# Performance work log

Hardware: AMD Instinct MI355X
Metric: run time of the kernel (lower is better)

The kernel has to match this reference:

```python
import jax, jax.numpy as jnp
import numpy as np
import math

VOCAB, D, H, NL, L, B = 50257, 768, 12, 4, 1024, 2
DH = D // H
DFF = 4 * D
ALPHA = 0.25
NEG = -1e9


def _ln(x, g, b, eps=1e-5):
    mu = x.mean(-1, keepdims=True)
    var = ((x - mu) ** 2).mean(-1, keepdims=True)
    return (x - mu) * jax.lax.rsqrt(var + eps) * g + b


def setup_inputs() -> dict:
    key = jax.random.key(0)
    ks = jax.random.split(key, 16)
    s = 0.02
    tokens = jax.random.randint(ks[0], (B, L), 0, VOCAB)
    timelike_mask = jax.random.randint(ks[1], (NL, D), 0, 2).astype(jnp.int32)
    embed = jax.random.normal(ks[2], (VOCAB, D), jnp.float32) * s
    pos_emb = jax.random.normal(ks[3], (L, D), jnp.float32) * s
    wq = jax.random.normal(ks[4], (NL, D, D), jnp.float32) * s
    wk = jax.random.normal(ks[5], (NL, D, D), jnp.float32) * s
    wv = jax.random.normal(ks[6], (NL, D, D), jnp.float32) * s
    wo = jax.random.normal(ks[7], (NL, D, D), jnp.float32) * s
    ff_w1 = jax.random.normal(ks[8], (NL, DFF, D), jnp.float32) * s
    ff_b1 = jnp.zeros((NL, DFF), jnp.float32)
    ff_w2 = jax.random.normal(ks[9], (NL, D, DFF), jnp.float32) * s
    ff_b2 = jnp.zeros((NL, D), jnp.float32)
    ln1_g = jnp.ones((NL, D), jnp.float32); ln1_b = jnp.zeros((NL, D), jnp.float32)
    ln2_g = jnp.ones((NL, D), jnp.float32); ln2_b = jnp.zeros((NL, D), jnp.float32)
    lnf_g = jnp.ones((D,), jnp.float32); lnf_b = jnp.zeros((D,), jnp.float32)
    return dict(tokens=tokens, timelike_mask=timelike_mask, embed=embed, pos_emb=pos_emb,
                wq=wq, wk=wk, wv=wv, wo=wo,
                ln1_g=ln1_g, ln1_b=ln1_b, ln2_g=ln2_g, ln2_b=ln2_b,
                ff_w1=ff_w1, ff_b1=ff_b1, ff_w2=ff_w2, ff_b2=ff_b2,
                lnf_g=lnf_g, lnf_b=lnf_b)


def reference(tokens, timelike_mask, embed, pos_emb, wq, wk, wv, wo,
              ln1_g, ln1_b, ln2_g, ln2_b, ff_w1, ff_b1, ff_w2, ff_b2,
              lnf_g, lnf_b):
    Bc, Lc = tokens.shape
    scale = math.sqrt(DH)
    # embeddings: token + learned position
    h = embed[tokens] + pos_emb[None, :Lc]  # (B,L,D)
    # additive causal mask, matching torch's -inf attention_mask convention
    causal = jnp.where(jnp.tril(jnp.ones((Lc, Lc), bool)), 0.0, NEG)[None, None]  # (1,1,L,L)
    for i in range(NL):
        xn = _ln(h, ln1_g[i], ln1_b[i])
        # nn.Linear(bias=False): y = x @ W.T, W is (out,in)
        q = jnp.einsum('bld,od->blo', xn, wq[i]).reshape(Bc, Lc, H, DH).astype(jnp.float32)
        k = jnp.einsum('bld,od->blo', xn, wk[i]).reshape(Bc, Lc, H, DH).astype(jnp.float32)
        v = jnp.einsum('bld,od->blo', xn, wv[i]).reshape(Bc, Lc, H, DH)
        # Minkowski term: scores_std - 2*alpha*(Q*P_t)K^T  ==  (Q*(1-2*alpha*m)) K^T
        m = timelike_mask[i].astype(jnp.float32).reshape(H, DH)  # per-head timelike directions
        q_eff = q * (1.0 - 2.0 * ALPHA * m)[None, None]
        scores = jnp.einsum('bqhd,bkhd->bhqk', q_eff, k) / scale + causal
        aw = jax.nn.softmax(scores, axis=-1)  # dropout=0 (eval)
        attn = jnp.einsum('bhqk,bkhd->bqhd', aw, v).reshape(Bc, Lc, D)
        h = h + jnp.einsum('bld,od->blo', attn, wo[i])
        xn2 = _ln(h, ln2_g[i], ln2_b[i])
        ff = jax.nn.gelu(jnp.einsum('bld,fd->blf', xn2, ff_w1[i]) + ff_b1[i], approximate=False)
        h = h + jnp.einsum('blf,df->bld', ff, ff_w2[i]) + ff_b2[i]
    h = _ln(h, lnf_g, lnf_b)
    logits = jnp.einsum('bld,vd->blv', h, embed)  # tied LM head
    return logits
```

## Files before the change

kernel.cpp:

```cpp
#include <hip/hip_runtime.h>
#include <math.h>

#define VOCABSZ 50257
#define VPAD 50432
#define DMODEL 768
#define NHEAD 12
#define NLAYER 4
#define SEQ 1024
#define BATCH 2
#define DHEAD 64
#define DFFN 3072
#define BT (BATCH * SEQ)
#define NBH (BATCH * NHEAD)

typedef __attribute__((ext_vector_type(8))) short bf16x8;
typedef __attribute__((ext_vector_type(4))) float f32x4;

__device__ __forceinline__ ushort f2bf(float f) {
  uint u = __builtin_bit_cast(uint, f);
  u = (u + 0x7fffu + ((u >> 16) & 1u)) >> 16;
  return (ushort)u;
}

__device__ __forceinline__ void gl_lds16(const ushort* g, ushort* l) {
  __builtin_amdgcn_global_load_lds(
      (const __attribute__((address_space(1))) void*)g,
      (__attribute__((address_space(3))) void*)l, 16, 0, 0);
}

__global__ __launch_bounds__(256) void conv4_kernel(
    const float* __restrict__ src, ushort* __restrict__ dst, int n4) {
  int i = blockIdx.x * 256 + threadIdx.x;
  if (i >= n4) return;
  float4 v = reinterpret_cast<const float4*>(src)[i];
  reinterpret_cast<ushort4*>(dst)[i] =
      make_ushort4(f2bf(v.x), f2bf(v.y), f2bf(v.z), f2bf(v.w));
}

__global__ __launch_bounds__(256) void conv_qkv_kernel(
    const float* __restrict__ src, ushort* __restrict__ dst, int qoff4) {
  const int per4 = DMODEL * DMODEL / 4;
  int i = blockIdx.x * 256 + threadIdx.x;
  if (i >= NLAYER * per4) return;
  int layer = i / per4, rem = i % per4;
  float4 v = reinterpret_cast<const float4*>(src)[i];
  reinterpret_cast<ushort4*>(dst)[(size_t)layer * (3 * per4) + qoff4 + rem] =
      make_ushort4(f2bf(v.x), f2bf(v.y), f2bf(v.z), f2bf(v.w));
}

__global__ __launch_bounds__(256) void conv_embed_kernel(
    const float* __restrict__ emb, ushort* __restrict__ dst) {
  int i = blockIdx.x * 256 + threadIdx.x;
  if (i >= VPAD * DMODEL / 4) return;
  int row = (i * 4) / DMODEL;
  ushort4 o = make_ushort4(0, 0, 0, 0);
  if (row < VOCABSZ) {
    float4 v = reinterpret_cast<const float4*>(emb)[i];
    o = make_ushort4(f2bf(v.x), f2bf(v.y), f2bf(v.z), f2bf(v.w));
  }
  reinterpret_cast<ushort4*>(dst)[i] = o;
}

__global__ __launch_bounds__(256) void embed_kernel(
    const int* __restrict__ tok, const float* __restrict__ emb,
    const float* __restrict__ pos, float* __restrict__ h) {
  int row = blockIdx.x;
  int l = row % SEQ;
  int t = tok[row];
  int tid = threadIdx.x;
#pragma unroll
  for (int j = 0; j < 3; ++j) {
    int c = tid + j * 256;
    h[(size_t)row * DMODEL + c] =
        emb[(size_t)t * DMODEL + c] + pos[(size_t)l * DMODEL + c];
  }
}

template <int KS, bool RBIAS>
__global__ __launch_bounds__(256) void ln_kernel(
    float* __restrict__ h, const float* __restrict__ part,
    const float* __restrict__ rb, const float* __restrict__ g,
    const float* __restrict__ bta, ushort* __restrict__ o) {
  __shared__ float red[8];
  int row = blockIdx.x;
  int tid = threadIdx.x;
  float* xr = h + (size_t)row * DMODEL;
  float v[3];
  float s = 0.f, sq = 0.f;
#pragma unroll
  for (int j = 0; j < 3; ++j) {
    int c = tid + j * 256;
    float a = xr[c];
    if (RBIAS) a += rb[c];
    if (KS > 0) {
#pragma unroll
      for (int z = 0; z < KS; ++z)
        a += part[(size_t)z * BT * DMODEL + (size_t)row * DMODEL + c];
      xr[c] = a;
    }
    v[j] = a;
    s += a;
    sq += a * a;
  }
#pragma unroll
  for (int off = 1; off < 64; off <<= 1) {
    s += __shfl_xor(s, off);
    sq += __shfl_xor(sq, off);
  }
  int wid = tid >> 6;
  if ((tid & 63) == 0) { red[wid * 2] = s; red[wid * 2 + 1] = sq; }
  __syncthreads();
  float S = red[0] + red[2] + red[4] + red[6];
  float SQ = red[1] + red[3] + red[5] + red[7];
  float mu = S * (1.0f / DMODEL);
  float var = SQ * (1.0f / DMODEL) - mu * mu;
  float r = rsqrtf(var + 1e-5f);
  ushort* orow = o + (size_t)row * DMODEL;
#pragma unroll
  for (int j = 0; j < 3; ++j) {
    int c = tid + j * 256;
    orow[c] = f2bf((v[j] - mu) * r * g[c] + bta[c]);
  }
}

__global__ __launch_bounds__(256) void fattn_kernel(
    const ushort* __restrict__ q, const ushort* __restrict__ k,
    const ushort* __restrict__ vt, ushort* __restrict__ o) {
  __shared__ __align__(16) ushort Ks[64 * 64];
  __shared__ __align__(16) ushort Vs[64 * 64];
  __shared__ __align__(16) ushort Ps[4][16][80];
  const int z = blockIdx.y, b = z / NHEAD, hh = z % NHEAD;
  const int q0 = (gridDim.x - 1 - blockIdx.x) * 64;
  const int tid = threadIdx.x, w = tid >> 6, l = tid & 63;
  const int fr = l & 15, ks = l >> 4;
  const int qrow = q0 + w * 16 + fr;
  const ushort* qp = q + (size_t)(b * SEQ + qrow) * DMODEL + hh * DHEAD;
  const bf16x8 qf0 = *reinterpret_cast<const bf16x8*>(qp + ks * 8);
  const bf16x8 qf1 = *reinterpret_cast<const bf16x8*>(qp + 32 + ks * 8);

  const int srow = w * 16 + (l >> 3);
  const int sslot = l & 7;

  f32x4 acc_o[4] = {};
  float mrun = -1e30f, lrun = 0.f;

  for (int k0 = 0; k0 <= q0; k0 += 64) {
#pragma unroll
    for (int c = 0; c < 2; ++c) {
      int r = srow + c * 8;
      int g = sslot ^ (r & 7);
      gl_lds16(k + (size_t)(b * SEQ + k0 + r) * DMODEL + hh * DHEAD + g * 8,
               Ks + (w * 16 + c * 8) * 64);
      gl_lds16(vt + (size_t)(z * 64 + r) * SEQ + k0 + g * 8,
               Vs + (w * 16 + c * 8) * 64);
    }
    __syncthreads();
    f32x4 acc_s[4] = {};
#pragma unroll
    for (int kstep = 0; kstep < 2; ++kstep) {
      const bf16x8 qf = kstep ? qf1 : qf0;
#pragma unroll
      for (int kb = 0; kb < 4; ++kb) {
        int ra = kb * 16 + fr;
        bf16x8 af = *reinterpret_cast<const bf16x8*>(
            Ks + ra * 64 + (((kstep * 4 + ks) ^ (ra & 7)) * 8));
        acc_s[kb] =
            __builtin_amdgcn_mfma_f32_16x16x32_bf16(af, qf, acc_s[kb], 0, 0, 0);
      }
    }
    const bool diag = (k0 == q0);
    float pm = -1e30f;
    float sv[4][4];
#pragma unroll
    for (int kb = 0; kb < 4; ++kb)
#pragma unroll
      for (int r = 0; r < 4; ++r) {
        float s = acc_s[kb][r];
        if (diag && (k0 + kb * 16 + ks * 4 + r > qrow)) s = -1e30f;
        sv[kb][r] = s;
        pm = fmaxf(pm, s);
      }
    pm = fmaxf(pm, __shfl_xor(pm, 16));
    pm = fmaxf(pm, __shfl_xor(pm, 32));
    float mnew = fmaxf(mrun, pm);
    float scale = __expf(mrun - mnew);
    float psum = 0.f;
#pragma unroll
    for (int kb = 0; kb < 4; ++kb) {
      float p0 = __expf(sv[kb][0] - mnew);
      float p1 = __expf(sv[kb][1] - mnew);
      float p2 = __expf(sv[kb][2] - mnew);
      float p3 = __expf(sv[kb][3] - mnew);
      psum += (p0 + p1) + (p2 + p3);
      *reinterpret_cast<ushort4*>(&Ps[w][fr][kb * 16 + ks * 4]) =
          make_ushort4(f2bf(p0), f2bf(p1), f2bf(p2), f2bf(p3));
    }
    psum += __shfl_xor(psum, 16);
    psum += __shfl_xor(psum, 32);
    lrun = lrun * scale + psum;
    mrun = mnew;
#pragma unroll
    for (int db = 0; db < 4; ++db) acc_o[db] *= scale;
#pragma unroll
    for (int kstep = 0; kstep < 2; ++kstep) {
      bf16x8 pf =
          *reinterpret_cast<const bf16x8*>(&Ps[w][fr][kstep * 32 + ks * 8]);
#pragma unroll
      for (int db = 0; db < 4; ++db) {
        int rd = db * 16 + fr;
        bf16x8 vf = *reinterpret_cast<const bf16x8*>(
            Vs + rd * 64 + (((kstep * 4 + ks) ^ (rd & 7)) * 8));
        acc_o[db] =
            __builtin_amdgcn_mfma_f32_16x16x32_bf16(vf, pf, acc_o[db], 0, 0, 0);
      }
    }
    __syncthreads();
  }
  float rinv = 1.0f / lrun;
#pragma unroll
  for (int db = 0; db < 4; ++db) {
    ushort4 o4 =
        make_ushort4(f2bf(acc_o[db][0] * rinv), f2bf(acc_o[db][1] * rinv),
                     f2bf(acc_o[db][2] * rinv), f2bf(acc_o[db][3] * rinv));
    *reinterpret_cast<ushort4*>(o + (size_t)(b * SEQ + qrow) * DMODEL +
                                hh * DHEAD + db * 16 + ks * 4) = o4;
  }
}

template <bool QKV, bool BIAS, bool GELU, bool RES, bool OUTBF, bool SWZ,
          bool PART>
__global__ __launch_bounds__(256) void gemm_bf16_nt(
    const ushort* __restrict__ A, const ushort* __restrict__ B,
    const float* __restrict__ bias, const int* __restrict__ tmask,
    const float* __restrict__ res, float* __restrict__ Cf,
    ushort* __restrict__ Cb, int ldc, ushort* __restrict__ qb,
    ushort* __restrict__ kb, ushort* __restrict__ vt, int M, int K, int Nreal,
    int kchunk) {
  __shared__ __align__(16) ushort As[2][128 * 32];
  __shared__ __align__(16) ushort Bs[2][128 * 32];
  int bnx, bmy;
  if (SWZ) {
    int bid = blockIdx.x;
    int chunk = gridDim.x >> 3;
    int wgid = (bid & 7) * chunk + (bid >> 3);
    int mb = M >> 7;
    bmy = wgid % mb;
    bnx = wgid / mb;
  } else {
    bnx = blockIdx.x;
    bmy = blockIdx.y;
  }
  const int m0 = bmy * 128, n0 = bnx * 128;
  const int kbeg = PART ? blockIdx.z * kchunk : 0;
  const int kend = PART ? kbeg + kchunk : K;
  if (PART) Cf += (size_t)blockIdx.z * M * ldc;
  const int tid = threadIdx.x;
  const int w = tid >> 6, l = tid & 63;
  const int wr = w >> 1, wc = w & 1;
  const int fr = l & 15, ks = l >> 4;

  const int seg0 = w * 2, seg1 = w * 2 + 1;
  const int srow0 = seg0 * 16 + (l >> 2);
  const int srow1 = seg1 * 16 + (l >> 2);
  const int koff0 = (((l & 3) ^ ((srow0 >> 1) & 3))) * 8;
  const int koff1 = (((l & 3) ^ ((srow1 >> 1) & 3))) * 8;
  const ushort* A0 = A + (size_t)(m0 + srow0) * K + koff0;
  const ushort* A1 = A + (size_t)(m0 + srow1) * K + koff1;
  const ushort* B0 = B + (size_t)(n0 + srow0) * K + koff0;
  const ushort* B1 = B + (size_t)(n0 + srow1) * K + koff1;

  int aoff[4], boff[4];
#pragma unroll
  for (int i = 0; i < 4; ++i) {
    int ra = wr * 64 + i * 16 + fr;
    aoff[i] = ra * 32 + ((ks ^ ((ra >> 1) & 3)) * 8);
    int rb = wc * 64 + i * 16 + fr;
    boff[i] = rb * 32 + ((ks ^ ((rb >> 1) & 3)) * 8);
  }

  gl_lds16(A0 + kbeg, &As[0][seg0 * 512]);
  gl_lds16(A1 + kbeg, &As[0][seg1 * 512]);
  gl_lds16(B0 + kbeg, &Bs[0][seg0 * 512]);
  gl_lds16(B1 + kbeg, &Bs[0][seg1 * 512]);

  f32x4 acc[4][4] = {};
  int cur = 0;
  for (int k0 = kbeg; k0 < kend; k0 += 32) {
    const int nxt = k0 + 32;
    if (nxt < kend) {
      gl_lds16(A0 + nxt, &As[cur ^ 1][seg0 * 512]);
      gl_lds16(A1 + nxt, &As[cur ^ 1][seg1 * 512]);
      gl_lds16(B0 + nxt, &Bs[cur ^ 1][seg0 * 512]);
      gl_lds16(B1 + nxt, &Bs[cur ^ 1][seg1 * 512]);
      asm volatile("s_waitcnt vmcnt(4)" ::: "memory");
    } else {
      asm volatile("s_waitcnt vmcnt(0)" ::: "memory");
    }
    __builtin_amdgcn_s_barrier();
    __builtin_amdgcn_sched_barrier(0);
    bf16x8 af[4], bfr[4];
#pragma unroll
    for (int i = 0; i < 4; ++i)
      af[i] = *reinterpret_cast<const bf16x8*>(&As[cur][aoff[i]]);
#pragma unroll
    for (int i = 0; i < 4; ++i)
      bfr[i] = *reinterpret_cast<const bf16x8*>(&Bs[cur][boff[i]]);
#pragma unroll
    for (int mi = 0; mi < 4; ++mi)
#pragma unroll
      for (int nj = 0; nj < 4; ++nj)
        acc[mi][nj] = __builtin_amdgcn_mfma_f32_16x16x32_bf16(
            af[mi], bfr[nj], acc[mi][nj], 0, 0, 0);
    __builtin_amdgcn_sched_barrier(0);
    __builtin_amdgcn_s_barrier();
    cur ^= 1;
  }

#pragma unroll
  for (int mi = 0; mi < 4; ++mi) {
#pragma unroll
    for (int nj = 0; nj < 4; ++nj) {
      int n = n0 + wc * 64 + nj * 16 + fr;
      if (n < Nreal) {
        if (PART) {
#pragma unroll
          for (int r = 0; r < 4; ++r) {
            int m = m0 + wr * 64 + mi * 16 + ks * 4 + r;
            Cf[(size_t)m * ldc + n] = acc[mi][nj][r];
          }
        } else if (QKV) {
          if (n < DMODEL) {
            float sc = (1.0f - 0.5f * (float)tmask[n]) * 0.125f;
#pragma unroll
            for (int r = 0; r < 4; ++r) {
              int m = m0 + wr * 64 + mi * 16 + ks * 4 + r;
              qb[(size_t)m * DMODEL + n] = f2bf(acc[mi][nj][r] * sc);
            }
          } else if (n < 2 * DMODEL) {
#pragma unroll
            for (int r = 0; r < 4; ++r) {
              int m = m0 + wr * 64 + mi * 16 + ks * 4 + r;
              kb[(size_t)m * DMODEL + (n - DMODEL)] = f2bf(acc[mi][nj][r]);
            }
          } else {
            int d = n - 2 * DMODEL;
            int key = (m0 & (SEQ - 1)) + wr * 64 + mi * 16 + ks * 4;
            size_t zr = (size_t)((m0 >> 10) * NHEAD + (d >> 6)) * 64 + (d & 63);
            ushort4 p4 = make_ushort4(
                f2bf(acc[mi][nj][0]), f2bf(acc[mi][nj][1]),
                f2bf(acc[mi][nj][2]), f2bf(acc[mi][nj][3]));
            *reinterpret_cast<ushort4*>(vt + zr * SEQ + key) = p4;
          }
        } else {
#pragma unroll
          for (int r = 0; r < 4; ++r) {
            int m = m0 + wr * 64 + mi * 16 + ks * 4 + r;
            float v = acc[mi][nj][r];
            if (BIAS) v += bias[n];
            if (GELU) v = 0.5f * v * (1.0f + erff(v * 0.70710678118f));
            if (RES) v += res[(size_t)m * ldc + n];
            if (OUTBF)
              Cb[(size_t)m * ldc + n] = f2bf(v);
            else
              Cf[(size_t)m * ldc + n] = v;
          }
        }
      }
    }
  }
}

extern "C" void kernel_launch(void* const* d_in, const int* in_sizes, int n_in,
                              void* d_out, int out_size, void* d_ws,
                              size_t ws_size, hipStream_t stream) {
  const int* tokens = (const int*)d_in[0];
  const int* tmask = (const int*)d_in[1];
  const float* embed = (const float*)d_in[2];
  const float* pos = (const float*)d_in[3];
  const float* wq = (const float*)d_in[4];
  const float* wk = (const float*)d_in[5];
  const float* wv = (const float*)d_in[6];
  const float* wo = (const float*)d_in[7];
  const float* ln1g = (const float*)d_in[8];
  const float* ln1b = (const float*)d_in[9];
  const float* ln2g = (const float*)d_in[10];
  const float* ln2b = (const float*)d_in[11];
  const float* fw1 = (const float*)d_in[12];
  const float* fb1 = (const float*)d_in[13];
  const float* fw2 = (const float*)d_in[14];
  const float* fb2 = (const float*)d_in[15];
  const float* lnfg = (const float*)d_in[16];
  const float* lnfb = (const float*)d_in[17];

  char* wp = (char*)d_ws;
  auto alloc = [&](size_t bytes) {
    void* p = wp;
    wp += (bytes + 255) & ~(size_t)255;
    return p;
  };
  float* h = (float*)alloc((size_t)BT * DMODEL * 4);
  float* part = (float*)alloc((size_t)4 * BT * DMODEL * 4);
  ushort* qb = (ushort*)alloc((size_t)BT * DMODEL * 2);
  ushort* kb = (ushort*)alloc((size_t)BT * DMODEL * 2);
  ushort* vt = (ushort*)alloc((size_t)NBH * DHEAD * SEQ * 2);
  ushort* xn = (ushort*)alloc((size_t)BT * DMODEL * 2);
  ushort* ab = (ushort*)alloc((size_t)BT * DMODEL * 2);
  ushort* ffb = (ushort*)alloc((size_t)BT * DFFN * 2);
  ushort* wqkv_b = (ushort*)alloc((size_t)NLAYER * 3 * DMODEL * DMODEL * 2);
  ushort* wo_b = (ushort*)alloc((size_t)NLAYER * DMODEL * DMODEL * 2);
  ushort* fw1_b = (ushort*)alloc((size_t)NLAYER * DFFN * DMODEL * 2);
  ushort* fw2_b = (ushort*)alloc((size_t)NLAYER * DMODEL * DFFN * 2);
  ushort* emb_b = (ushort*)alloc((size_t)VPAD * DMODEL * 2);

  const int per4 = DMODEL * DMODEL / 4;
  conv_qkv_kernel<<<(NLAYER * per4 + 255) / 256, 256, 0, stream>>>(wq, wqkv_b, 0);
  conv_qkv_kernel<<<(NLAYER * per4 + 255) / 256, 256, 0, stream>>>(wk, wqkv_b, per4);
  conv_qkv_kernel<<<(NLAYER * per4 + 255) / 256, 256, 0, stream>>>(wv, wqkv_b, 2 * per4);
  conv4_kernel<<<(NLAYER * per4 + 255) / 256, 256, 0, stream>>>(wo, wo_b, NLAYER * per4);
  const int nff4 = NLAYER * DFFN * DMODEL / 4;
  conv4_kernel<<<(nff4 + 255) / 256, 256, 0, stream>>>(fw1, fw1_b, nff4);
  conv4_kernel<<<(nff4 + 255) / 256, 256, 0, stream>>>(fw2, fw2_b, nff4);
  conv_embed_kernel<<<(VPAD * DMODEL / 4 + 255) / 256, 256, 0, stream>>>(embed, emb_b);

  embed_kernel<<<BT, 256, 0, stream>>>(tokens, embed, pos, h);

  const dim3 gqkv(3 * DMODEL / 128, BT / 128);
  const dim3 gff(DFFN / 128, BT / 128);
  const dim3 gwo(DMODEL / 128, BT / 128, 2);
  const dim3 gff2(DMODEL / 128, BT / 128, 4);
  const int gv = (BT / 128) * (VPAD / 128);

  for (int i = 0; i < NLAYER; ++i) {
    if (i == 0)
      ln_kernel<0, false><<<BT, 256, 0, stream>>>(
          h, nullptr, nullptr, ln1g + i * DMODEL, ln1b + i * DMODEL, xn);
    else
      ln_kernel<4, true><<<BT, 256, 0, stream>>>(
          h, part, fb2 + (i - 1) * DMODEL, ln1g + i * DMODEL,
          ln1b + i * DMODEL, xn);

    gemm_bf16_nt<true, false, false, false, false, false, false>
        <<<gqkv, 256, 0, stream>>>(
            xn, wqkv_b + (size_t)i * 3 * DMODEL * DMODEL, nullptr,
            tmask + i * DMODEL, nullptr, nullptr, nullptr, 0, qb, kb, vt, BT,
            DMODEL, 3 * DMODEL, DMODEL);

    fattn_kernel<<<dim3(SEQ / 64, NBH), 256, 0, stream>>>(qb, kb, vt, ab);

    gemm_bf16_nt<false, false, false, false, false, false, true>
        <<<gwo, 256, 0, stream>>>(
            ab, wo_b + (size_t)i * DMODEL * DMODEL, nullptr, nullptr, nullptr,
            part, nullptr, DMODEL, nullptr, nullptr, nullptr, BT, DMODEL,
            DMODEL, DMODEL / 2);

    ln_kernel<2, false><<<BT, 256, 0, stream>>>(
        h, part, nullptr, ln2g + i * DMODEL, ln2b + i * DMODEL, xn);

    gemm_bf16_nt<false, true, true, false, true, false, false>
        <<<gff, 256, 0, stream>>>(
            xn, fw1_b + (size_t)i * DFFN * DMODEL, fb1 + i * DFFN, nullptr,
            nullptr, nullptr, ffb, DFFN, nullptr, nullptr, nullptr, BT, DMODEL,
            DFFN, DMODEL);

    gemm_bf16_nt<false, false, false, false, false, false, true>
        <<<gff2, 256, 0, stream>>>(
            ffb, fw2_b + (size_t)i * DMODEL * DFFN, nullptr, nullptr, nullptr,
            part, nullptr, DMODEL, nullptr, nullptr, nullptr, BT, DFFN, DMODEL,
            DFFN / 4);
  }

  ln_kernel<4, true><<<BT, 256, 0, stream>>>(
      h, part, fb2 + (NLAYER - 1) * DMODEL, lnfg, lnfb, xn);

  gemm_bf16_nt<false, false, false, false, false, true, false>
      <<<gv, 256, 0, stream>>>(
          xn, emb_b, nullptr, nullptr, nullptr, (float*)d_out, nullptr,
          VOCABSZ, nullptr, nullptr, nullptr, BT, DMODEL, VOCABSZ, DMODEL);
}
```

Measured before the change: 927.2 us.

## Double-buffer attention and add dedicated 256x256 LM-head GEMM with swizzled grids

Flash attention now double-buffers K/V tiles in LDS with explicit vmcnt waits, remaps its grid through an XCD-aware block swizzle, and skips the rescale of the running max unless it grows by more than a threshold. A new 512-thread LM-head GEMM with 256x256 tiles, double-buffered LDS loads and MFMA priority hints replaces the generic GEMM for the vocabulary projection. The QKV and FFN1 GEMMs switch to the swizzled 1D grid variant. These changes aim to hide global load latency and improve L2 locality, at the cost of more LDS and registers, which may lower occupancy.

```diff
diff --git a/kernel.cpp b/kernel.cpp
--- a/kernel.cpp
+++ b/kernel.cpp
@@ -126,11 +126,14 @@
 __global__ __launch_bounds__(256) void fattn_kernel(
     const ushort* __restrict__ q, const ushort* __restrict__ k,
     const ushort* __restrict__ vt, ushort* __restrict__ o) {
-  __shared__ __align__(16) ushort Ks[64 * 64];
-  __shared__ __align__(16) ushort Vs[64 * 64];
+  __shared__ __align__(16) ushort Ks[2][64 * 64];
+  __shared__ __align__(16) ushort Vs[2][64 * 64];
   __shared__ __align__(16) ushort Ps[4][16][80];
-  const int z = blockIdx.y, b = z / NHEAD, hh = z % NHEAD;
-  const int q0 = (gridDim.x - 1 - blockIdx.x) * 64;
+  const int bid = blockIdx.x;
+  const int wgid = (bid & 7) * 48 + (bid >> 3);
+  const int z = wgid / 16, qb_ = wgid % 16;
+  const int b = z / NHEAD, hh = z % NHEAD;
+  const int q0 = (15 - qb_) * 64;
   const int tid = threadIdx.x, w = tid >> 6, l = tid & 63;
   const int fr = l & 15, ks = l >> 4;
   const int qrow = q0 + w * 16 + fr;
@@ -139,23 +142,36 @@
   const bf16x8 qf1 = *reinterpret_cast<const bf16x8*>(qp + 32 + ks * 8);
 
   const int srow = w * 16 + (l >> 3);
-  const int sslot = l & 7;
+  const int g0 = ((l & 7) ^ (srow & 7)) * 8;
+
+  auto stage = [&](int k0, int d) {
+#pragma unroll
+    for (int c = 0; c < 2; ++c) {
+      int r = srow + c * 8;
+      gl_lds16(k + (size_t)(b * SEQ + k0 + r) * DMODEL + hh * DHEAD + g0,
+               &Ks[d][(w * 16 + c * 8) * 64]);
+      gl_lds16(vt + (size_t)(z * 64 + r) * SEQ + k0 + g0,
+               &Vs[d][(w * 16 + c * 8) * 64]);
+    }
+  };
 
   f32x4 acc_o[4] = {};
   float mrun = -1e30f, lrun = 0.f;
-
-  for (int k0 = 0; k0 <= q0; k0 += 64) {
-#pragma unroll
-    for (int c = 0; c < 2; ++c) {
-      int r = srow + c * 8;
-      int g = sslot ^ (r & 7);
-      gl_lds16(k + (size_t)(b * SEQ + k0 + r) * DMODEL + hh * DHEAD + g * 8,
-               Ks + (w * 16 + c * 8) * 64);
-      gl_lds16(vt + (size_t)(z * 64 + r) * SEQ + k0 + g * 8,
-               Vs + (w * 16 + c * 8) * 64);
-    }
-    __syncthreads();
+  const int nt = q0 >> 6;
+
+  stage(0, 0);
+  for (int t = 0; t <= nt; ++t) {
+    const int cur = t & 1;
+    if (t < nt) {
+      stage((t + 1) * 64, cur ^ 1);
+      asm volatile("s_waitcnt vmcnt(4)" ::: "memory");
+    } else {
+      asm volatile("s_waitcnt vmcnt(0)" ::: "memory");
+    }
+    __builtin_amdgcn_s_barrier();
+    __builtin_amdgcn_sched_barrier(0);
     f32x4 acc_s[4] = {};
+    __builtin_amdgcn_s_setprio(1);
 #pragma unroll
     for (int kstep = 0; kstep < 2; ++kstep) {
       const bf16x8 qf = kstep ? qf1 : qf0;
@@ -163,12 +179,13 @@
       for (int kb = 0; kb < 4; ++kb) {
         int ra = kb * 16 + fr;
         bf16x8 af = *reinterpret_cast<const bf16x8*>(
-            Ks + ra * 64 + (((kstep * 4 + ks) ^ (ra & 7)) * 8));
+            &Ks[cur][ra * 64 + (((kstep * 4 + ks) ^ (ra & 7)) * 8)]);
         acc_s[kb] =
             __builtin_amdgcn_mfma_f32_16x16x32_bf16(af, qf, acc_s[kb], 0, 0, 0);
       }
     }
-    const bool diag = (k0 == q0);
+    __builtin_amdgcn_s_setprio(0);
+    const bool diag = (t == nt);
     float pm = -1e30f;
     float sv[4][4];
 #pragma unroll
@@ -176,31 +193,35 @@
 #pragma unroll
       for (int r = 0; r < 4; ++r) {
         float s = acc_s[kb][r];
-        if (diag && (k0 + kb * 16 + ks * 4 + r > qrow)) s = -1e30f;
+        if (diag && (q0 + kb * 16 + ks * 4 + r > qrow)) s = -1e30f;
         sv[kb][r] = s;
         pm = fmaxf(pm, s);
       }
     pm = fmaxf(pm, __shfl_xor(pm, 16));
     pm = fmaxf(pm, __shfl_xor(pm, 32));
-    float mnew = fmaxf(mrun, pm);
-    float scale = __expf(mrun - mnew);
+    if (!__all(pm - mrun <= 8.0f)) {
+      float mnew = fmaxf(mrun, pm);
+      float scale = __expf(mrun - mnew);
+      lrun *= scale;
+#pragma unroll
+      for (int db = 0; db < 4; ++db) acc_o[db] *= scale;
+      mrun = mnew;
+    }
     float psum = 0.f;
 #pragma unroll
     for (int kb = 0; kb < 4; ++kb) {
-      float p0 = __expf(sv[kb][0] - mnew);
-      float p1 = __expf(sv[kb][1] - mnew);
-      float p2 = __expf(sv[kb][2] - mnew);
-      float p3 = __expf(sv[kb][3] - mnew);
+      float p0 = __expf(sv[kb][0] - mrun);
+      float p1 = __expf(sv[kb][1] - mrun);
+      float p2 = __expf(sv[kb][2] - mrun);
+      float p3 = __expf(sv[kb][3] - mrun);
       psum += (p0 + p1) + (p2 + p3);
       *reinterpret_cast<ushort4*>(&Ps[w][fr][kb * 16 + ks * 4]) =
           make_ushort4(f2bf(p0), f2bf(p1), f2bf(p2), f2bf(p3));
     }
     psum += __shfl_xor(psum, 16);
     psum += __shfl_xor(psum, 32);
-    lrun = lrun * scale + psum;
-    mrun = mnew;
-#pragma unroll
-    for (int db = 0; db < 4; ++db) acc_o[db] *= scale;
+    lrun += psum;
+    __builtin_amdgcn_s_setprio(1);
 #pragma unroll
     for (int kstep = 0; kstep < 2; ++kstep) {
       bf16x8 pf =
@@ -209,12 +230,14 @@
       for (int db = 0; db < 4; ++db) {
         int rd = db * 16 + fr;
         bf16x8 vf = *reinterpret_cast<const bf16x8*>(
-            Vs + rd * 64 + (((kstep * 4 + ks) ^ (rd & 7)) * 8));
+            &Vs[cur][rd * 64 + (((kstep * 4 + ks) ^ (rd & 7)) * 8)]);
         acc_o[db] =
             __builtin_amdgcn_mfma_f32_16x16x32_bf16(vf, pf, acc_o[db], 0, 0, 0);
       }
     }
-    __syncthreads();
+    __builtin_amdgcn_s_setprio(0);
+    __builtin_amdgcn_sched_barrier(0);
+    __builtin_amdgcn_s_barrier();
   }
   float rinv = 1.0f / lrun;
 #pragma unroll
@@ -370,6 +393,104 @@
   }
 }
 
+__global__ __launch_bounds__(512, 2) void gemm_lmhead(
+    const ushort* __restrict__ A, const ushort* __restrict__ B,
+    float* __restrict__ C) {
+  __shared__ __align__(16) ushort As[2][256 * 64];
+  __shared__ __align__(16) ushort Bs[2][256 * 64];
+  const int K = DMODEL;
+  const int NT = K / 64;
+
+  const int bid = blockIdx.x;
+  const int chunk = gridDim.x >> 3;
+  const int wgid = (bid & 7) * chunk + (bid >> 3);
+  const int m0 = (wgid & 7) * 256;
+  const int n0 = (wgid >> 3) * 256;
+
+  const int tid = threadIdx.x;
+  const int w = tid >> 6, l = tid & 63;
+  const int wr = w >> 2, wc = w & 3;
+  const int fr = l & 15, ks = l >> 4;
+
+  const int srow = tid >> 3;
+  const int skoff = ((tid & 7) ^ ((tid >> 3) & 7)) * 8;
+
+  int aoff[8][2], boff[4][2];
+#pragma unroll
+  for (int mi = 0; mi < 8; ++mi) {
+    int ra = wr * 128 + mi * 16 + fr;
+#pragma unroll
+    for (int kst = 0; kst < 2; ++kst)
+      aoff[mi][kst] = ra * 64 + (((kst * 4 + ks) ^ (ra & 7)) * 8);
+  }
+#pragma unroll
+  for (int nj = 0; nj < 4; ++nj) {
+    int rb = wc * 64 + nj * 16 + fr;
+#pragma unroll
+    for (int kst = 0; kst < 2; ++kst)
+      boff[nj][kst] = rb * 64 + (((kst * 4 + ks) ^ (rb & 7)) * 8);
+  }
+
+  auto stage = [&](int t, int d) {
+#pragma unroll
+    for (int c = 0; c < 4; ++c)
+      gl_lds16(A + (size_t)(m0 + c * 64 + srow) * K + t * 64 + skoff,
+               &As[d][c * 4096 + w * 512]);
+#pragma unroll
+    for (int c = 0; c < 4; ++c)
+      gl_lds16(B + (size_t)(n0 + c * 64 + srow) * K + t * 64 + skoff,
+               &Bs[d][c * 4096 + w * 512]);
+  };
+
+  f32x4 acc[8][4] = {};
+  stage(0, 0);
+  int cur = 0;
+  for (int t = 0; t < NT; ++t) {
+    if (t + 1 < NT) {
+      stage(t + 1, cur ^ 1);
+      asm volatile("s_waitcnt vmcnt(8)" ::: "memory");
+    } else {
+      asm volatile("s_waitcnt vmcnt(0)" ::: "memory");
+    }
+    __builtin_amdgcn_s_barrier();
+    __builtin_amdgcn_sched_barrier(0);
+#pragma unroll
+    for (int kst = 0; kst < 2; ++kst) {
+      bf16x8 bfr[4];
+#pragma unroll
+      for (int nj = 0; nj < 4; ++nj)
+        bfr[nj] = *reinterpret_cast<const bf16x8*>(&Bs[cur][boff[nj][kst]]);
+      __builtin_amdgcn_s_setprio(1);
+#pragma unroll
+      for (int mi = 0; mi < 8; ++mi) {
+        bf16x8 af = *reinterpret_cast<const bf16x8*>(&As[cur][aoff[mi][kst]]);
+#pragma unroll
+        for (int nj = 0; nj < 4; ++nj)
+          acc[mi][nj] = __builtin_amdgcn_mfma_f32_16x16x32_bf16(
+              af, bfr[nj], acc[mi][nj], 0, 0, 0);
+      }
+      __builtin_amdgcn_s_setprio(0);
+    }
+    __builtin_amdgcn_sched_barrier(0);
+    __builtin_amdgcn_s_barrier();
+    cur ^= 1;
+  }
+
+#pragma unroll
+  for (int mi = 0; mi < 8; ++mi) {
+#pragma unroll
+    for (int nj = 0; nj < 4; ++nj) {
+      int n = n0 + wc * 64 + nj * 16 + fr;
+      if (n < VOCABSZ) {
+        int m = m0 + wr * 128 + mi * 16 + ks * 4;
+#pragma unroll
+        for (int r = 0; r < 4; ++r)
+          C[(size_t)(m + r) * VOCABSZ + n] = acc[mi][nj][r];
+      }
+    }
+  }
+}
+
 extern "C" void kernel_launch(void* const* d_in, const int* in_sizes, int n_in,
                               void* d_out, int out_size, void* d_ws,
                               size_t ws_size, hipStream_t stream) {
@@ -424,11 +545,10 @@
 
   embed_kernel<<<BT, 256, 0, stream>>>(tokens, embed, pos, h);
 
-  const dim3 gqkv(3 * DMODEL / 128, BT / 128);
-  const dim3 gff(DFFN / 128, BT / 128);
+  const int gqkv = (3 * DMODEL / 128) * (BT / 128);
+  const int gff = (DFFN / 128) * (BT / 128);
   const dim3 gwo(DMODEL / 128, BT / 128, 2);
   const dim3 gff2(DMODEL / 128, BT / 128, 4);
-  const int gv = (BT / 128) * (VPAD / 128);
 
   for (int i = 0; i < NLAYER; ++i) {
     if (i == 0)
@@ -439,13 +559,13 @@
           h, part, fb2 + (i - 1) * DMODEL, ln1g + i * DMODEL,
           ln1b + i * DMODEL, xn);
 
-    gemm_bf16_nt<true, false, false, false, false, false, false>
+    gemm_bf16_nt<true, false, false, false, false, true, false>
         <<<gqkv, 256, 0, stream>>>(
             xn, wqkv_b + (size_t)i * 3 * DMODEL * DMODEL, nullptr,
             tmask + i * DMODEL, nullptr, nullptr, nullptr, 0, qb, kb, vt, BT,
             DMODEL, 3 * DMODEL, DMODEL);
 
-    fattn_kernel<<<dim3(SEQ / 64, NBH), 256, 0, stream>>>(qb, kb, vt, ab);
+    fattn_kernel<<<NBH * (SEQ / 64), 256, 0, stream>>>(qb, kb, vt, ab);
 
     gemm_bf16_nt<false, false, false, false, false, false, true>
         <<<gwo, 256, 0, stream>>>(
@@ -456,7 +576,7 @@
     ln_kernel<2, false><<<BT, 256, 0, stream>>>(
         h, part, nullptr, ln2g + i * DMODEL, ln2b + i * DMODEL, xn);
 
-    gemm_bf16_nt<false, true, true, false, true, false, false>
+    gemm_bf16_nt<false, true, true, false, true, true, false>
         <<<gff, 256, 0, stream>>>(
             xn, fw1_b + (size_t)i * DFFN * DMODEL, fb1 + i * DFFN, nullptr,
             nullptr, nullptr, ffb, DFFN, nullptr, nullptr, nullptr, BT, DMODEL,
@@ -472,8 +592,5 @@
   ln_kernel<4, true><<<BT, 256, 0, stream>>>(
       h, part, fb2 + (NLAYER - 1) * DMODEL, lnfg, lnfb, xn);
 
-  gemm_bf16_nt<false, false, false, false, false, true, false>
-      <<<gv, 256, 0, stream>>>(
-          xn, emb_b, nullptr, nullptr, nullptr, (float*)d_out, nullptr,
-          VOCABSZ, nullptr, nullptr, nullptr, BT, DMODEL, VOCABSZ, DMODEL);
-}
+  gemm_lmhead<<<8 * (VPAD / 256), 512, 0, stream>>>(xn, emb_b, (float*)d_out);
+}
```

Result: no change. 945.6 us (+2.0%).
